# Optimization experiments

Hardware: AMD Instinct MI355X
Metric: run time of the kernel (lower is better)

Reference implementation:

```python
import jax, jax.numpy as jnp
import numpy as np
from jax import lax

B, H, E = 32, 2050, 128        # batch, input height, num_emb (conv width)
N = 2048                        # num_nodes = H - (kernel_size - 1)
C = 128                         # hidden_channels_CNN[0]
G1, G2 = 128, 128               # hidden_channels_GNN
MLP = 100                       # hidden_channels_MLP
OUT = 1                         # output_dim
KS = 3                          # kernel_size
NE = 32768                      # num edges


def setup_inputs() -> dict:
    key = jax.random.key(0)
    ks = jax.random.split(key, 12)
    s = 0.02
    inp = {
        "x": jax.random.normal(ks[0], (B, H, E), dtype=jnp.float32),
        "edge_index": jax.random.randint(ks[1], (2, NE), 0, N, dtype=jnp.int64),
        # Conv2d(1, C, kernel=(KS, E)) -> OIHW weight [C, 1, KS, E]
        "conv_w": jax.random.normal(ks[2], (C, 1, KS, E), dtype=jnp.float32) * s,
        "conv_b": jax.random.normal(ks[3], (C,), dtype=jnp.float32) * s,
        # GCNConv weights (linear has no bias; bias added after aggregation)
        "gW1": jax.random.normal(ks[4], (C, G1), dtype=jnp.float32) * s,
        "gb1": jax.random.normal(ks[5], (G1,), dtype=jnp.float32) * s,
        "gW2": jax.random.normal(ks[6], (G1, G2), dtype=jnp.float32) * s,
        "gb2": jax.random.normal(ks[7], (G2,), dtype=jnp.float32) * s,
        "W1": jax.random.normal(ks[8], (G2 * N, MLP), dtype=jnp.float32) * s,
        "b1": jax.random.normal(ks[9], (MLP,), dtype=jnp.float32) * s,
        "W2": jax.random.normal(ks[10], (MLP, OUT), dtype=jnp.float32) * s,
        "b2": jax.random.normal(ks[11], (OUT,), dtype=jnp.float32) * s,
    }
    return inp


def _gcn_norm(edge_index, n):
    # PyG gcn_norm with add_self_loops=True, edge_weight = 1
    loops = jnp.arange(n, dtype=edge_index.dtype)
    src = jnp.concatenate([edge_index[0], loops])
    dst = jnp.concatenate([edge_index[1], loops])
    deg = jax.ops.segment_sum(jnp.ones_like(dst, dtype=jnp.float32), dst, num_segments=n)
    dinv = jnp.where(deg > 0, lax.rsqrt(jnp.maximum(deg, 1.0)), 0.0)
    norm = dinv[src] * dinv[dst]
    return src, dst, norm


def _gcn_layer(h, src, dst, norm, W, b):
    # h: [B, N, Fin] -> out[b, dst] = sum_e norm_e * (h @ W)[b, src_e] + b
    hw = h @ W                                   # [B, N, Fout]
    msgs = hw[:, src, :] * norm[None, :, None]    # [B, E+N, Fout]
    agg = jnp.zeros_like(hw).at[:, dst, :].add(msgs)
    return agg + b


def reference(x, edge_index, conv_w, conv_b, gW1, gb1, gW2, gb2, W1, b1, W2, b2):
    # CNN feature extraction: [B,1,H,E] conv (KS,E) -> [B,C,N,1]
    x4 = x[:, None, :, :]
    h = lax.conv_general_dilated(x4, conv_w, window_strides=(1, 1), padding='VALID',
                                 dimension_numbers=('NCHW', 'OIHW', 'NCHW'))
    h = jax.nn.relu(h + conv_b[None, :, None, None])
    h = jnp.transpose(h[:, :, :, 0], (0, 2, 1))   # [B, N, C]

    src, dst, norm = _gcn_norm(edge_index, N)
    h = jax.nn.relu(_gcn_layer(h, src, dst, norm, gW1, gb1))
    h = jax.nn.relu(_gcn_layer(h, src, dst, norm, gW2, gb2))

    h = h.reshape(B, -1)                          # [B, N*G2]
    h = jax.nn.relu(h @ W1 + b1)
    # dropout: eval mode (identity)
    out = h @ W2 + b2
    return out.astype(jnp.float32)
```

## Files before the change

kernel.cpp:

```cpp
#include <hip/hip_runtime.h>
#include <stdint.h>

typedef unsigned short u16;
typedef __attribute__((ext_vector_type(8))) short bf16x8;
typedef __attribute__((ext_vector_type(4))) float f32x4;

#define NN 2048
#define NEDGE 32768
#define NBLK 1024
#define KC 256
#define NRG 4
#define PW 112

__device__ __forceinline__ float bf2f(uint32_t u) {
  union { uint32_t i; float f; } c; c.i = u << 16; return c.f;
}
__device__ __forceinline__ uint32_t f2bf(float f) {
  union { float f; uint32_t i; } c; c.f = f;
  uint32_t x = c.i;
  return (x + 0x7fffu + ((x >> 16) & 1u)) >> 16;
}

__global__ void k_prep(const float4* __restrict__ cw, uint2* __restrict__ wtb,
                       const float* __restrict__ g1, const float* __restrict__ g2,
                       u16* __restrict__ o1, u16* __restrict__ o2,
                       int* __restrict__ cnt, int* __restrict__ cursor) {
  int blk = blockIdx.x;
  if (blk < 48) {
    int i = blk * 256 + threadIdx.x;
    float4 v = cw[i];
    uint2 o;
    o.x = f2bf(v.x) | (f2bf(v.y) << 16);
    o.y = f2bf(v.z) | (f2bf(v.w) << 16);
    wtb[i] = o;
  } else if (blk < 112) {
    int i = (blk - 48) * 256 + threadIdx.x;
    int r = i >> 7, c = i & 127;
    o1[i] = (u16)f2bf(g1[c * 128 + r]);
    o2[i] = (u16)f2bf(g2[c * 128 + r]);
  } else {
    int i = (blk - 112) * 256 + threadIdx.x;
    cnt[i] = 1; cursor[i] = 0;
  }
}

__global__ void k_count(const int* __restrict__ edge, int* __restrict__ cnt) {
  int i = blockIdx.x * 256 + threadIdx.x;
  if (i < NEDGE) atomicAdd(&cnt[edge[NEDGE + i]], 1);
}

__global__ __launch_bounds__(1024) void k_scan(const int* __restrict__ cnt, int* __restrict__ rowp) {
  __shared__ int s[1024];
  int t = threadIdx.x;
  int c0 = cnt[2 * t], c1 = cnt[2 * t + 1];
  s[t] = c0 + c1;
  __syncthreads();
  for (int off = 1; off < 1024; off <<= 1) {
    int v = (t >= off) ? s[t - off] : 0;
    __syncthreads();
    s[t] += v;
    __syncthreads();
  }
  int excl = s[t] - c0 - c1;
  rowp[2 * t] = excl;
  rowp[2 * t + 1] = excl + c0;
  if (t == 1023) rowp[2048] = s[t];
}

__global__ void k_fill(const int* __restrict__ edge, const int* __restrict__ cnt,
                       const int* __restrict__ rowp, int* __restrict__ cursor,
                       int* __restrict__ colx, float* __restrict__ wgt) {
  int i = blockIdx.x * 256 + threadIdx.x;
  if (i >= NEDGE + NN) return;
  int s, d;
  if (i < NEDGE) { s = edge[i]; d = edge[NEDGE + i]; }
  else { s = i - NEDGE; d = s; }
  float wv = rsqrtf((float)cnt[s] * (float)cnt[d]);
  int pos = atomicAdd(&cursor[d], 1);
  int idx = rowp[d] + pos;
  colx[idx] = s;
  wgt[idx] = wv;
}

__global__ __launch_bounds__(256) void k_gemmf(
    const float* __restrict__ A, const u16* __restrict__ Bt,
    const float* __restrict__ bias, u16* __restrict__ C,
    int K, int bExtra)
{
  __shared__ u16 lA[128 * 64];
  __shared__ u16 lB[128 * 64];
  const int t = threadIdx.x;
  const int Mbase = blockIdx.x * 128;
  const size_t aBase = (size_t)Mbase * 128 + (size_t)(Mbase >> 11) * bExtra;
  const int w = t >> 6, l = t & 63;
  const int wrM = (w >> 1) * 64, wrN = (w & 1) * 64;
  const int lm = l & 15, lkh = l >> 4;
  const int rph0 = t >> 3, pc = t & 7;
  const int rt2 = t >> 1, hf = t & 1;
  f32x4 acc[4][4];
#pragma unroll
  for (int i = 0; i < 4; ++i)
#pragma unroll
    for (int j = 0; j < 4; ++j)
      acc[i][j] = (f32x4){0.f, 0.f, 0.f, 0.f};

  for (int kc = 0; kc < K; kc += 64) {
    __syncthreads();
#pragma unroll
    for (int it = 0; it < 4; ++it) {
      int r = it * 32 + rph0;
      int lc = pc ^ (r & 7);
      char* dstB = (char*)lB + it * 4096 + w * 1024;
      __builtin_amdgcn_global_load_lds(
          (const void*)(Bt + (size_t)r * K + kc + lc * 8), dstB, 16, 0, 0);
    }
    {
      const float4* src = (const float4*)(A + aBase + (size_t)rt2 * 128 + kc + hf * 32);
      float4 f[8];
#pragma unroll
      for (int c = 0; c < 8; ++c) f[c] = src[c];
#pragma unroll
      for (int cc = 0; cc < 4; ++cc) {
        uint4 pk;
        pk.x = f2bf(f[2 * cc].x)     | (f2bf(f[2 * cc].y) << 16);
        pk.y = f2bf(f[2 * cc].z)     | (f2bf(f[2 * cc].w) << 16);
        pk.z = f2bf(f[2 * cc + 1].x) | (f2bf(f[2 * cc + 1].y) << 16);
        pk.w = f2bf(f[2 * cc + 1].z) | (f2bf(f[2 * cc + 1].w) << 16);
        int ch = hf * 4 + cc;
        *(uint4*)((char*)lA + rt2 * 128 + ((ch ^ (rt2 & 7)) << 4)) = pk;
      }
    }
    __syncthreads();
#pragma unroll
    for (int kk = 0; kk < 2; ++kk) {
      int lc = kk * 4 + lkh;
      bf16x8 af[4], bfr[4];
#pragma unroll
      for (int i = 0; i < 4; ++i) {
        int R = wrM + i * 16 + lm;
        af[i] = *(const bf16x8*)((const char*)lA + R * 128 + ((lc ^ (R & 7)) << 4));
      }
#pragma unroll
      for (int j = 0; j < 4; ++j) {
        int R = wrN + j * 16 + lm;
        bfr[j] = *(const bf16x8*)((const char*)lB + R * 128 + ((lc ^ (R & 7)) << 4));
      }
#pragma unroll
      for (int i = 0; i < 4; ++i)
#pragma unroll
        for (int j = 0; j < 4; ++j)
          acc[i][j] = __builtin_amdgcn_mfma_f32_16x16x32_bf16(af[i], bfr[j], acc[i][j], 0, 0, 0);
    }
  }
  const int rq = (l >> 4) * 4;
#pragma unroll
  for (int i = 0; i < 4; ++i) {
#pragma unroll
    for (int j = 0; j < 4; ++j) {
      int col = wrN + j * 16 + lm;
      float bv = bias[col];
#pragma unroll
      for (int q = 0; q < 4; ++q) {
        int row = Mbase + wrM + i * 16 + rq + q;
        float v = acc[i][j][q] + bv;
        v = fmaxf(v, 0.f);
        C[(size_t)row * 128 + col] = (u16)f2bf(v);
      }
    }
  }
}

__global__ __launch_bounds__(256) void k_gemm(
    const u16* __restrict__ A, const u16* __restrict__ Bt,
    const float* __restrict__ bias, u16* __restrict__ C,
    int K)
{
  __shared__ u16 lA[128 * 64];
  __shared__ u16 lB[128 * 64];
  const int t = threadIdx.x;
  const int Mbase = blockIdx.x * 128;
  const size_t aBase = (size_t)Mbase * 128;
  const int w = t >> 6, l = t & 63;
  const int wrM = (w >> 1) * 64, wrN = (w & 1) * 64;
  const int lm = l & 15, lkh = l >> 4;
  const int rph0 = t >> 3, pc = t & 7;
  f32x4 acc[4][4];
#pragma unroll
  for (int i = 0; i < 4; ++i)
#pragma unroll
    for (int j = 0; j < 4; ++j)
      acc[i][j] = (f32x4){0.f, 0.f, 0.f, 0.f};

  for (int kc = 0; kc < K; kc += 64) {
    __syncthreads();
#pragma unroll
    for (int it = 0; it < 4; ++it) {
      int r = it * 32 + rph0;
      int lc = pc ^ (r & 7);
      char* dstA = (char*)lA + it * 4096 + w * 1024;
      char* dstB = (char*)lB + it * 4096 + w * 1024;
      __builtin_amdgcn_global_load_lds(
          (const void*)(A + aBase + (size_t)r * 128 + kc + lc * 8), dstA, 16, 0, 0);
      __builtin_amdgcn_global_load_lds(
          (const void*)(Bt + (size_t)r * K + kc + lc * 8), dstB, 16, 0, 0);
    }
    __syncthreads();
#pragma unroll
    for (int kk = 0; kk < 2; ++kk) {
      int lc = kk * 4 + lkh;
      bf16x8 af[4], bfr[4];
#pragma unroll
      for (int i = 0; i < 4; ++i) {
        int R = wrM + i * 16 + lm;
        af[i] = *(const bf16x8*)((const char*)lA + R * 128 + ((lc ^ (R & 7)) << 4));
      }
#pragma unroll
      for (int j = 0; j < 4; ++j) {
        int R = wrN + j * 16 + lm;
        bfr[j] = *(const bf16x8*)((const char*)lB + R * 128 + ((lc ^ (R & 7)) << 4));
      }
#pragma unroll
      for (int i = 0; i < 4; ++i)
#pragma unroll
        for (int j = 0; j < 4; ++j)
          acc[i][j] = __builtin_amdgcn_mfma_f32_16x16x32_bf16(af[i], bfr[j], acc[i][j], 0, 0, 0);
    }
  }
  const int rq = (l >> 4) * 4;
#pragma unroll
  for (int i = 0; i < 4; ++i) {
#pragma unroll
    for (int j = 0; j < 4; ++j) {
      int col = wrN + j * 16 + lm;
      float bv = bias[col];
#pragma unroll
      for (int q = 0; q < 4; ++q) {
        int row = Mbase + wrM + i * 16 + rq + q;
        float v = acc[i][j][q] + bv;
        v = fmaxf(v, 0.f);
        C[(size_t)row * 128 + col] = (u16)f2bf(v);
      }
    }
  }
}

__global__ __launch_bounds__(256) void k_gather(
    const u16* __restrict__ h, const int* __restrict__ rowp,
    const int* __restrict__ colx, const float* __restrict__ wgt,
    u16* __restrict__ out)
{
  int w = threadIdx.x >> 6, l = threadIdx.x & 63;
  int bid = blockIdx.x;
  int sb = (bid & 7) * 2048 + (bid >> 3);
  int p = sb * 4 + w;
  int b = p >> 11, v = p & 2047;
  int e0 = rowp[v], e1 = rowp[v + 1];
  const u16* hb = h + (size_t)b * (2048 * 128);
  float a0 = 0.f, a1 = 0.f;
  int e = e0;
  for (; e + 8 <= e1; e += 8) {
    int u0 = colx[e], u1 = colx[e + 1], u2 = colx[e + 2], u3 = colx[e + 3];
    int u4 = colx[e + 4], u5 = colx[e + 5], u6 = colx[e + 6], u7 = colx[e + 7];
    float w0 = wgt[e], w1 = wgt[e + 1], w2 = wgt[e + 2], w3 = wgt[e + 3];
    float w4 = wgt[e + 4], w5 = wgt[e + 5], w6 = wgt[e + 6], w7 = wgt[e + 7];
    uint32_t k0 = *(const uint32_t*)(hb + (size_t)u0 * 128 + l * 2);
    uint32_t k1 = *(const uint32_t*)(hb + (size_t)u1 * 128 + l * 2);
    uint32_t k2 = *(const uint32_t*)(hb + (size_t)u2 * 128 + l * 2);
    uint32_t k3 = *(const uint32_t*)(hb + (size_t)u3 * 128 + l * 2);
    uint32_t k4 = *(const uint32_t*)(hb + (size_t)u4 * 128 + l * 2);
    uint32_t k5 = *(const uint32_t*)(hb + (size_t)u5 * 128 + l * 2);
    uint32_t k6 = *(const uint32_t*)(hb + (size_t)u6 * 128 + l * 2);
    uint32_t k7 = *(const uint32_t*)(hb + (size_t)u7 * 128 + l * 2);
    a0 += w0 * bf2f(k0 & 0xffffu) + w1 * bf2f(k1 & 0xffffu)
        + w2 * bf2f(k2 & 0xffffu) + w3 * bf2f(k3 & 0xffffu)
        + w4 * bf2f(k4 & 0xffffu) + w5 * bf2f(k5 & 0xffffu)
        + w6 * bf2f(k6 & 0xffffu) + w7 * bf2f(k7 & 0xffffu);
    a1 += w0 * bf2f(k0 >> 16) + w1 * bf2f(k1 >> 16)
        + w2 * bf2f(k2 >> 16) + w3 * bf2f(k3 >> 16)
        + w4 * bf2f(k4 >> 16) + w5 * bf2f(k5 >> 16)
        + w6 * bf2f(k6 >> 16) + w7 * bf2f(k7 >> 16);
  }
  for (; e + 4 <= e1; e += 4) {
    int u0 = colx[e], u1 = colx[e + 1], u2 = colx[e + 2], u3 = colx[e + 3];
    float w0 = wgt[e], w1 = wgt[e + 1], w2 = wgt[e + 2], w3 = wgt[e + 3];
    uint32_t k0 = *(const uint32_t*)(hb + (size_t)u0 * 128 + l * 2);
    uint32_t k1 = *(const uint32_t*)(hb + (size_t)u1 * 128 + l * 2);
    uint32_t k2 = *(const uint32_t*)(hb + (size_t)u2 * 128 + l * 2);
    uint32_t k3 = *(const uint32_t*)(hb + (size_t)u3 * 128 + l * 2);
    a0 += w0 * bf2f(k0 & 0xffffu) + w1 * bf2f(k1 & 0xffffu)
        + w2 * bf2f(k2 & 0xffffu) + w3 * bf2f(k3 & 0xffffu);
    a1 += w0 * bf2f(k0 >> 16) + w1 * bf2f(k1 >> 16)
        + w2 * bf2f(k2 >> 16) + w3 * bf2f(k3 >> 16);
  }
  for (; e < e1; ++e) {
    int u = colx[e];
    float wv = wgt[e];
    uint32_t pk = *(const uint32_t*)(hb + (size_t)u * 128 + l * 2);
    a0 += wv * bf2f(pk & 0xffffu);
    a1 += wv * bf2f(pk >> 16);
  }
  uint32_t o = f2bf(a0) | (f2bf(a1) << 16);
  *(uint32_t*)(out + (size_t)p * 128 + l * 2) = o;
}

__global__ __launch_bounds__(256) void k_mlp1(
    const u16* __restrict__ h3, const float* __restrict__ W1, float* __restrict__ part)
{
  __shared__ u16 sA[32][264];
  __shared__ u16 sB[112][264];
  const int t = threadIdx.x;
  const int blk = blockIdx.x;
  const int j0 = blk * KC;
  {
    int r = t >> 3, c = (t & 7) * 32;
    const u16* src = h3 + (size_t)r * 262144 + j0 + c;
#pragma unroll
    for (int u = 0; u < 4; ++u)
      *(bf16x8*)&sA[r][c + u * 8] = *(const bf16x8*)(src + u * 8);
  }
  for (int it = 0; it < 13; ++it) {
    int task = it * 256 + t;
    if (task < 3200) {
      int jp = task / 25, mq = task % 25;
      const float* wp = W1 + (size_t)(j0 + 2 * jp) * 100 + mq * 4;
      float4 fa = *(const float4*)wp;
      float4 fb = *(const float4*)(wp + 100);
      uint32_t p0 = f2bf(fa.x) | (f2bf(fb.x) << 16);
      uint32_t p1 = f2bf(fa.y) | (f2bf(fb.y) << 16);
      uint32_t p2 = f2bf(fa.z) | (f2bf(fb.z) << 16);
      uint32_t p3 = f2bf(fa.w) | (f2bf(fb.w) << 16);
      int m = mq * 4;
      *(uint32_t*)&sB[m + 0][2 * jp] = p0;
      *(uint32_t*)&sB[m + 1][2 * jp] = p1;
      *(uint32_t*)&sB[m + 2][2 * jp] = p2;
      *(uint32_t*)&sB[m + 3][2 * jp] = p3;
    }
  }
  __syncthreads();
  const int w = t >> 6, l = t & 63;
  const int mt = w >> 1, nh = w & 1;
  const int nt0 = nh * 4, ntn = nh ? 3 : 4;
  const int lm = l & 15, lk8 = (l >> 4) * 8;
  f32x4 acc[4];
#pragma unroll
  for (int n = 0; n < 4; ++n) acc[n] = (f32x4){0.f, 0.f, 0.f, 0.f};
#pragma unroll
  for (int kk = 0; kk < 8; ++kk) {
    int ko = kk * 32 + lk8;
    bf16x8 af = *(const bf16x8*)&sA[mt * 16 + lm][ko];
#pragma unroll
    for (int n = 0; n < 4; ++n) {
      if (n < ntn) {
        bf16x8 bfr = *(const bf16x8*)&sB[(nt0 + n) * 16 + lm][ko];
        acc[n] = __builtin_amdgcn_mfma_f32_16x16x32_bf16(af, bfr, acc[n], 0, 0, 0);
      }
    }
  }
  const int rq = (l >> 4) * 4;
#pragma unroll
  for (int n = 0; n < 4; ++n) {
    if (n < ntn) {
      int m = (nt0 + n) * 16 + lm;
#pragma unroll
      for (int q = 0; q < 4; ++q) {
        int b = mt * 16 + rq + q;
        part[((size_t)blk * 32 + b) * PW + m] = acc[n][q];
      }
    }
  }
}

__global__ __launch_bounds__(256) void k_red(
    const float* __restrict__ part, float* __restrict__ part2)
{
  int e = blockIdx.x * 256 + threadIdx.x;
  int rg = blockIdx.y;
  const float* p = part + (size_t)rg * 256 * (32 * PW) + e;
  float s0 = 0.f, s1 = 0.f, s2 = 0.f, s3 = 0.f;
  for (int r = 0; r < 256; r += 4) {
    s0 += p[(size_t)(r + 0) * (32 * PW)];
    s1 += p[(size_t)(r + 1) * (32 * PW)];
    s2 += p[(size_t)(r + 2) * (32 * PW)];
    s3 += p[(size_t)(r + 3) * (32 * PW)];
  }
  part2[rg * (32 * PW) + e] = (s0 + s1) + (s2 + s3);
}

__global__ __launch_bounds__(128) void k_mlp2(
    const float* __restrict__ part2, const float* __restrict__ b1,
    const float* __restrict__ W2, const float* __restrict__ b2, float* __restrict__ out)
{
  __shared__ float sh[100];
  int b = blockIdx.x, t = threadIdx.x;
  if (t < 100) {
    float s = 0.f;
#pragma unroll
    for (int rg = 0; rg < NRG; ++rg)
      s += part2[rg * (32 * PW) + b * PW + t];
    float h = fmaxf(s + b1[t], 0.f);
    sh[t] = h * W2[t];
  }
  __syncthreads();
  if (t == 0) {
    float s = 0.f;
    for (int m = 0; m < 100; ++m) s += sh[m];
    out[b] = s + b2[0];
  }
}

extern "C" void kernel_launch(void* const* d_in, const int* in_sizes, int n_in,
                              void* d_out, int out_size, void* d_ws, size_t ws_size,
                              hipStream_t stream) {
  (void)in_sizes; (void)n_in; (void)out_size; (void)ws_size;
  const float* x      = (const float*)d_in[0];
  const int* edge     = (const int*)d_in[1];
  const float* conv_w = (const float*)d_in[2];
  const float* conv_b = (const float*)d_in[3];
  const float* gW1    = (const float*)d_in[4];
  const float* gb1    = (const float*)d_in[5];
  const float* gW2    = (const float*)d_in[6];
  const float* gb2    = (const float*)d_in[7];
  const float* W1     = (const float*)d_in[8];
  const float* b1     = (const float*)d_in[9];
  const float* W2     = (const float*)d_in[10];
  const float* b2     = (const float*)d_in[11];
  float* out = (float*)d_out;

  char* ws = (char*)d_ws;
  size_t off = 0;
  auto alloc = [&](size_t bytes) {
    void* p = ws + off;
    off = (off + bytes + 255) & ~(size_t)255;
    return p;
  };
  u16* bufA   = (u16*)alloc(8388608ull * 2);
  u16* bufB   = (u16*)alloc(8388608ull * 2);
  u16* Wtb    = (u16*)alloc(49152ull * 2);
  u16* g1t    = (u16*)alloc(16384ull * 2);
  u16* g2t    = (u16*)alloc(16384ull * 2);
  int* cnt    = (int*)alloc(2048 * 4);
  int* cursor = (int*)alloc(2048 * 4);
  int* rowp   = (int*)alloc(2052 * 4);
  int* colx   = (int*)alloc(34816 * 4);
  float* wgt  = (float*)alloc(34816 * 4);
  float* part = (float*)alloc((size_t)NBLK * 32 * PW * 4);
  float* part2= (float*)alloc((size_t)NRG * (32 * PW) * 4);

  k_prep<<<120, 256, 0, stream>>>((const float4*)conv_w, (uint2*)Wtb,
                                  gW1, gW2, g1t, g2t, cnt, cursor);
  k_count<<<128, 256, 0, stream>>>(edge, cnt);
  k_scan<<<1, 1024, 0, stream>>>(cnt, rowp);
  k_fill<<<(NEDGE + NN + 255) / 256, 256, 0, stream>>>(edge, cnt, rowp, cursor, colx, wgt);

  k_gemmf<<<512, 256, 0, stream>>>(x, Wtb, conv_b, bufA, 384, 256);
  k_gather<<<16384, 256, 0, stream>>>(bufA, rowp, colx, wgt, bufB);
  k_gemm<<<512, 256, 0, stream>>>(bufB, g1t, gb1, bufA, 128);
  k_gather<<<16384, 256, 0, stream>>>(bufA, rowp, colx, wgt, bufB);
  k_gemm<<<512, 256, 0, stream>>>(bufB, g2t, gb2, bufA, 128);
  k_mlp1<<<NBLK, 256, 0, stream>>>(bufA, W1, part);
  k_red<<<dim3(14, NRG), 256, 0, stream>>>(part, part2);
  k_mlp2<<<32, 128, 0, stream>>>(part2, b1, W2, b2, out);
}
```

Before: 186.4 us.

## Switch GNN activations to node-major layout for wide contiguous gathers

Stores the activations node-major, as [node][batch][channel], instead of batch-major. The first GEMM epilogue writes rows in the remapped order, and the MLP1 loader reads this layout. The gather kernel now uses one block per destination node covering all 32 batches, so each neighbour fetch becomes a contiguous 8 KB read done with 16-byte loads. This is meant to cut the narrow scattered 4-byte loads and the repeated reads of edge index and weight data for every batch. In exchange, each thread keeps 16 accumulators and the grid is much smaller.

```diff
diff --git a/kernel.cpp b/kernel.cpp
--- a/kernel.cpp
+++ b/kernel.cpp
@@ -19,6 +19,17 @@
   union { float f; uint32_t i; } c; c.f = f;
   uint32_t x = c.i;
   return (x + 0x7fffu + ((x >> 16) & 1u)) >> 16;
+}
+
+__device__ __forceinline__ void fma8(float* acc, uint4 q, float wv) {
+  acc[0] += wv * bf2f(q.x & 0xffffu);
+  acc[1] += wv * bf2f(q.x >> 16);
+  acc[2] += wv * bf2f(q.y & 0xffffu);
+  acc[3] += wv * bf2f(q.y >> 16);
+  acc[4] += wv * bf2f(q.z & 0xffffu);
+  acc[5] += wv * bf2f(q.z >> 16);
+  acc[6] += wv * bf2f(q.w & 0xffffu);
+  acc[7] += wv * bf2f(q.w >> 16);
 }
 
 __global__ void k_prep(const float4* __restrict__ cw, uint2* __restrict__ wtb,
@@ -161,10 +172,11 @@
       float bv = bias[col];
 #pragma unroll
       for (int q = 0; q < 4; ++q) {
-        int row = Mbase + wrM + i * 16 + rq + q;
+        int g = Mbase + wrM + i * 16 + rq + q;
+        int orow = ((g & 2047) << 5) | (g >> 11);
         float v = acc[i][j][q] + bv;
         v = fmaxf(v, 0.f);
-        C[(size_t)row * 128 + col] = (u16)f2bf(v);
+        C[(size_t)orow * 128 + col] = (u16)f2bf(v);
       }
     }
   }
@@ -244,63 +256,51 @@
   }
 }
 
-__global__ __launch_bounds__(256) void k_gather(
+__global__ __launch_bounds__(256) void k_gatherT(
     const u16* __restrict__ h, const int* __restrict__ rowp,
     const int* __restrict__ colx, const float* __restrict__ wgt,
     u16* __restrict__ out)
 {
-  int w = threadIdx.x >> 6, l = threadIdx.x & 63;
-  int bid = blockIdx.x;
-  int sb = (bid & 7) * 2048 + (bid >> 3);
-  int p = sb * 4 + w;
-  int b = p >> 11, v = p & 2047;
-  int e0 = rowp[v], e1 = rowp[v + 1];
-  const u16* hb = h + (size_t)b * (2048 * 128);
-  float a0 = 0.f, a1 = 0.f;
+  const int t = threadIdx.x;
+  const int v = blockIdx.x;
+  const int b = t >> 3, cg = t & 7;
+  const int e0 = rowp[v], e1 = rowp[v + 1];
+  float acc[16];
+#pragma unroll
+  for (int i = 0; i < 16; ++i) acc[i] = 0.f;
   int e = e0;
-  for (; e + 8 <= e1; e += 8) {
-    int u0 = colx[e], u1 = colx[e + 1], u2 = colx[e + 2], u3 = colx[e + 3];
-    int u4 = colx[e + 4], u5 = colx[e + 5], u6 = colx[e + 6], u7 = colx[e + 7];
-    float w0 = wgt[e], w1 = wgt[e + 1], w2 = wgt[e + 2], w3 = wgt[e + 3];
-    float w4 = wgt[e + 4], w5 = wgt[e + 5], w6 = wgt[e + 6], w7 = wgt[e + 7];
-    uint32_t k0 = *(const uint32_t*)(hb + (size_t)u0 * 128 + l * 2);
-    uint32_t k1 = *(const uint32_t*)(hb + (size_t)u1 * 128 + l * 2);
-    uint32_t k2 = *(const uint32_t*)(hb + (size_t)u2 * 128 + l * 2);
-    uint32_t k3 = *(const uint32_t*)(hb + (size_t)u3 * 128 + l * 2);
-    uint32_t k4 = *(const uint32_t*)(hb + (size_t)u4 * 128 + l * 2);
-    uint32_t k5 = *(const uint32_t*)(hb + (size_t)u5 * 128 + l * 2);
-    uint32_t k6 = *(const uint32_t*)(hb + (size_t)u6 * 128 + l * 2);
-    uint32_t k7 = *(const uint32_t*)(hb + (size_t)u7 * 128 + l * 2);
-    a0 += w0 * bf2f(k0 & 0xffffu) + w1 * bf2f(k1 & 0xffffu)
-        + w2 * bf2f(k2 & 0xffffu) + w3 * bf2f(k3 & 0xffffu)
-        + w4 * bf2f(k4 & 0xffffu) + w5 * bf2f(k5 & 0xffffu)
-        + w6 * bf2f(k6 & 0xffffu) + w7 * bf2f(k7 & 0xffffu);
-    a1 += w0 * bf2f(k0 >> 16) + w1 * bf2f(k1 >> 16)
-        + w2 * bf2f(k2 >> 16) + w3 * bf2f(k3 >> 16)
-        + w4 * bf2f(k4 >> 16) + w5 * bf2f(k5 >> 16)
-        + w6 * bf2f(k6 >> 16) + w7 * bf2f(k7 >> 16);
-  }
-  for (; e + 4 <= e1; e += 4) {
-    int u0 = colx[e], u1 = colx[e + 1], u2 = colx[e + 2], u3 = colx[e + 3];
-    float w0 = wgt[e], w1 = wgt[e + 1], w2 = wgt[e + 2], w3 = wgt[e + 3];
-    uint32_t k0 = *(const uint32_t*)(hb + (size_t)u0 * 128 + l * 2);
-    uint32_t k1 = *(const uint32_t*)(hb + (size_t)u1 * 128 + l * 2);
-    uint32_t k2 = *(const uint32_t*)(hb + (size_t)u2 * 128 + l * 2);
-    uint32_t k3 = *(const uint32_t*)(hb + (size_t)u3 * 128 + l * 2);
-    a0 += w0 * bf2f(k0 & 0xffffu) + w1 * bf2f(k1 & 0xffffu)
-        + w2 * bf2f(k2 & 0xffffu) + w3 * bf2f(k3 & 0xffffu);
-    a1 += w0 * bf2f(k0 >> 16) + w1 * bf2f(k1 >> 16)
-        + w2 * bf2f(k2 >> 16) + w3 * bf2f(k3 >> 16);
+  for (; e + 2 <= e1; e += 2) {
+    int u0 = colx[e], u1 = colx[e + 1];
+    float w0 = wgt[e], w1 = wgt[e + 1];
+    const uint4* p0 = (const uint4*)(h + ((size_t)u0 * 32 + b) * 128 + cg * 16);
+    const uint4* p1 = (const uint4*)(h + ((size_t)u1 * 32 + b) * 128 + cg * 16);
+    uint4 qa0 = p0[0], qa1 = p0[1];
+    uint4 qb0 = p1[0], qb1 = p1[1];
+    fma8(acc, qa0, w0);
+    fma8(acc + 8, qa1, w0);
+    fma8(acc, qb0, w1);
+    fma8(acc + 8, qb1, w1);
   }
   for (; e < e1; ++e) {
     int u = colx[e];
     float wv = wgt[e];
-    uint32_t pk = *(const uint32_t*)(hb + (size_t)u * 128 + l * 2);
-    a0 += wv * bf2f(pk & 0xffffu);
-    a1 += wv * bf2f(pk >> 16);
-  }
-  uint32_t o = f2bf(a0) | (f2bf(a1) << 16);
-  *(uint32_t*)(out + (size_t)p * 128 + l * 2) = o;
+    const uint4* p = (const uint4*)(h + ((size_t)u * 32 + b) * 128 + cg * 16);
+    uint4 q0 = p[0], q1 = p[1];
+    fma8(acc, q0, wv);
+    fma8(acc + 8, q1, wv);
+  }
+  uint4 o0, o1;
+  o0.x = f2bf(acc[0])  | (f2bf(acc[1])  << 16);
+  o0.y = f2bf(acc[2])  | (f2bf(acc[3])  << 16);
+  o0.z = f2bf(acc[4])  | (f2bf(acc[5])  << 16);
+  o0.w = f2bf(acc[6])  | (f2bf(acc[7])  << 16);
+  o1.x = f2bf(acc[8])  | (f2bf(acc[9])  << 16);
+  o1.y = f2bf(acc[10]) | (f2bf(acc[11]) << 16);
+  o1.z = f2bf(acc[12]) | (f2bf(acc[13]) << 16);
+  o1.w = f2bf(acc[14]) | (f2bf(acc[15]) << 16);
+  uint4* dst = (uint4*)(out + ((size_t)v * 32 + b) * 128 + cg * 16);
+  dst[0] = o0;
+  dst[1] = o1;
 }
 
 __global__ __launch_bounds__(256) void k_mlp1(
@@ -312,11 +312,13 @@
   const int blk = blockIdx.x;
   const int j0 = blk * KC;
   {
-    int r = t >> 3, c = (t & 7) * 32;
-    const u16* src = h3 + (size_t)r * 262144 + j0 + c;
+    int r = t >> 3, q = t & 7;
+    int v = (j0 >> 7) + (q >> 2);
+    int d = (q & 3) * 32;
+    const u16* src = h3 + ((size_t)v * 32 + r) * 128 + d;
 #pragma unroll
     for (int u = 0; u < 4; ++u)
-      *(bf16x8*)&sA[r][c + u * 8] = *(const bf16x8*)(src + u * 8);
+      *(bf16x8*)&sA[r][q * 32 + u * 8] = *(const bf16x8*)(src + u * 8);
   }
   for (int it = 0; it < 13; ++it) {
     int task = it * 256 + t;
@@ -453,9 +455,9 @@
   k_fill<<<(NEDGE + NN + 255) / 256, 256, 0, stream>>>(edge, cnt, rowp, cursor, colx, wgt);
 
   k_gemmf<<<512, 256, 0, stream>>>(x, Wtb, conv_b, bufA, 384, 256);
-  k_gather<<<16384, 256, 0, stream>>>(bufA, rowp, colx, wgt, bufB);
+  k_gatherT<<<2048, 256, 0, stream>>>(bufA, rowp, colx, wgt, bufB);
   k_gemm<<<512, 256, 0, stream>>>(bufB, g1t, gb1, bufA, 128);
-  k_gather<<<16384, 256, 0, stream>>>(bufA, rowp, colx, wgt, bufB);
+  k_gatherT<<<2048, 256, 0, stream>>>(bufA, rowp, colx, wgt, bufB);
   k_gemm<<<512, 256, 0, stream>>>(bufB, g2t, gb2, bufA, 128);
   k_mlp1<<<NBLK, 256, 0, stream>>>(bufA, W1, part);
   k_red<<<dim3(14, NRG), 256, 0, stream>>>(part, part2);
```

After: 189.6 us. No clear change (+1.7%).
